# Optimization experiments

Measured on AMD Instinct MI355X. Metric: run time of the kernel, lower is better.

## Reference

```python
import jax, jax.numpy as jnp
import numpy as np

D = H = W = 128
C = 16
VOXEL_SIZE = 0.05  # origin = 0, grid spans [0, 6.4]^3 in world coords
N_POINTS = 2_000_000


def setup_inputs() -> dict:
    key = jax.random.key(0)
    k1, k2 = jax.random.split(key)
    # world-space query points uniformly inside the grid bounds
    points = jax.random.uniform(k1, (N_POINTS, 3), dtype=jnp.float32) * (D * VOXEL_SIZE)
    values = jax.random.normal(k2, (D, H, W, C), dtype=jnp.float32)
    return {"points": points, "values": values}


def reference(points, values):
    # world -> grid coords (origin = 0)
    gc = points / VOXEL_SIZE  # [N, 3]
    x, y, z = gc[:, 0], gc[:, 1], gc[:, 2]

    x0 = jnp.clip(jnp.floor(x).astype(jnp.int32), 0, D - 1)
    y0 = jnp.clip(jnp.floor(y).astype(jnp.int32), 0, H - 1)
    z0 = jnp.clip(jnp.floor(z).astype(jnp.int32), 0, W - 1)
    x1 = jnp.clip(x0 + 1, 0, D - 1)
    y1 = jnp.clip(y0 + 1, 0, H - 1)
    z1 = jnp.clip(z0 + 1, 0, W - 1)

    # fractional offsets (computed against the clipped floor index, as in source)
    xd = (x - x0.astype(x.dtype))[:, None]
    yd = (y - y0.astype(y.dtype))[:, None]
    zd = (z - z0.astype(z.dtype))[:, None]

    # flatten grid for efficient single-axis gather
    flat = values.reshape(D * H * W, C)

    def gather(xi, yi, zi):
        lin = (xi * H + yi) * W + zi  # [N]
        return jnp.take(flat, lin, axis=0)  # [N, C]

    c000 = gather(x0, y0, z0)
    c001 = gather(x0, y0, z1)
    c010 = gather(x0, y1, z0)
    c011 = gather(x0, y1, z1)
    c100 = gather(x1, y0, z0)
    c101 = gather(x1, y0, z1)
    c110 = gather(x1, y1, z0)
    c111 = gather(x1, y1, z1)

    c00 = c000 * (1 - xd) + c100 * xd
    c01 = c001 * (1 - xd) + c101 * xd
    c10 = c010 * (1 - xd) + c110 * xd
    c11 = c011 * (1 - xd) + c111 * xd
    c0 = c00 * (1 - yd) + c10 * yd
    c1 = c01 * (1 - yd) + c11 * yd
    return c0 * (1 - zd) + c1 * zd  # [N, C]
```

## Files before the change

### kernel.cpp

```cpp
#include <hip/hip_runtime.h>


#define DD 128
#define HH 128
#define WW 128
#define NBX 16
#define NB (NBX * NBX * NBX)
#define NPART 4
#define CAP2 152
#define CUR_STRIDE 16

typedef float fvec4 __attribute__((ext_vector_type(4)));

__device__ __forceinline__ float4 lerp4(float4 a, float4 b, float t) {
    return make_float4(fmaf(b.x - a.x, t, a.x),
                       fmaf(b.y - a.y, t, a.y),
                       fmaf(b.z - a.z, t, a.z),
                       fmaf(b.w - a.w, t, a.w));
}

__device__ __forceinline__ int clampi(int v, int lo, int hi) {
    return min(max(v, lo), hi);
}

__device__ __forceinline__ float4 trilerp_point(const float4* __restrict__ values,
                                                float x, float y, float z, int c4) {
    float fx = floorf(x), fy = floorf(y), fz = floorf(z);
    int x0 = clampi((int)fx, 0, DD - 1);
    int y0 = clampi((int)fy, 0, HH - 1);
    int z0 = clampi((int)fz, 0, WW - 1);
    int x1 = min(x0 + 1, DD - 1);
    int y1 = min(y0 + 1, HH - 1);
    int z1 = min(z0 + 1, WW - 1);

    float xd = x - (float)x0;
    float yd = y - (float)y0;
    float zd = z - (float)z0;

    #define VIDX(xi, yi, zi) ((((((xi) << 7) + (yi)) << 7) + (zi)) * 4 + c4)
    float4 c000 = values[VIDX(x0, y0, z0)];
    float4 c001 = values[VIDX(x0, y0, z1)];
    float4 c010 = values[VIDX(x0, y1, z0)];
    float4 c011 = values[VIDX(x0, y1, z1)];
    float4 c100 = values[VIDX(x1, y0, z0)];
    float4 c101 = values[VIDX(x1, y0, z1)];
    float4 c110 = values[VIDX(x1, y1, z0)];
    float4 c111 = values[VIDX(x1, y1, z1)];
    #undef VIDX

    float4 c00 = lerp4(c000, c100, xd);
    float4 c01 = lerp4(c001, c101, xd);
    float4 c10 = lerp4(c010, c110, xd);
    float4 c11 = lerp4(c011, c111, xd);
    float4 c0  = lerp4(c00, c10, yd);
    float4 c1  = lerp4(c01, c11, yd);
    return lerp4(c0, c1, zd);
}

__global__ __launch_bounds__(256) void scatter_kernel(
    const float* __restrict__ points,
    unsigned* __restrict__ cursors,
    float4* __restrict__ recs,
    const float4* __restrict__ values,
    float4* __restrict__ out,
    int n_points)
{
    int p = blockIdx.x * blockDim.x + threadIdx.x;
    if (p >= n_points) return;
    int part = blockIdx.x & (NPART - 1);

    float x = points[p * 3 + 0] * 20.0f;
    float y = points[p * 3 + 1] * 20.0f;
    float z = points[p * 3 + 2] * 20.0f;

    int bx = clampi((int)floorf(x), 0, DD - 1) >> 3;
    int by = clampi((int)floorf(y), 0, HH - 1) >> 3;
    int bz = clampi((int)floorf(z), 0, WW - 1) >> 3;
    int sb = (part * NB) + ((bx * NBX + by) * NBX + bz);

    unsigned pos = atomicAdd(&cursors[sb * CUR_STRIDE], 1u);
    if (pos < CAP2) {
        fvec4 r = { x, y, z, __uint_as_float((unsigned)p) };
        __builtin_nontemporal_store(r, (fvec4*)(recs + (size_t)sb * CAP2 + pos));
    } else {
        #pragma unroll
        for (int c = 0; c < 4; ++c)
            out[p * 4 + c] = trilerp_point(values, x, y, z, c);
    }
}

__global__ __launch_bounds__(256) void interp_kernel(
    const float4* __restrict__ recs,
    const unsigned* __restrict__ cursors,
    const float4* __restrict__ values,
    float4* __restrict__ out)
{
    __shared__ float4 sv[9 * 9 * 9 * 4];

    int b = blockIdx.x;
    int bz = b & 15, by = (b >> 4) & 15, bx = b >> 8;
    int X0 = bx << 3, Y0 = by << 3, Z0 = bz << 3;

    for (int e = threadIdx.x; e < 9 * 9 * 9 * 4; e += 256) {
        int v = e >> 2, c = e & 3;
        int i = v / 81;
        int r = v - i * 81;
        int j = r / 9;
        int k = r - j * 9;
        int gx = min(X0 + i, DD - 1);
        int gy = min(Y0 + j, HH - 1);
        int gz = min(Z0 + k, WW - 1);
        sv[e] = values[((((gx << 7) + gy) << 7) + gz) * 4 + c];
    }
    __syncthreads();

    int c4 = threadIdx.x & 3;

    #define SIDX(i, j, k) (((((i) * 9) + (j)) * 9 + (k)) * 4 + c4)
    for (int part = 0; part < NPART; ++part) {
        int sb = part * NB + b;
        unsigned cnt = cursors[sb * CUR_STRIDE];
        if (cnt > CAP2) cnt = CAP2;
        const float4* rp = recs + (size_t)sb * CAP2;

        for (unsigned j = threadIdx.x >> 2; j < cnt; j += 64) {
            float4 r = rp[j];
            float x = r.x, y = r.y, z = r.z;

            float fx = floorf(x), fy = floorf(y), fz = floorf(z);
            int x0 = clampi((int)fx, 0, DD - 1);
            int y0 = clampi((int)fy, 0, HH - 1);
            int z0 = clampi((int)fz, 0, WW - 1);
            float xd = x - (float)x0;
            float yd = y - (float)y0;
            float zd = z - (float)z0;

            int xl = x0 - X0, yl = y0 - Y0, zl = z0 - Z0;
            float4 c000 = sv[SIDX(xl,     yl,     zl    )];
            float4 c001 = sv[SIDX(xl,     yl,     zl + 1)];
            float4 c010 = sv[SIDX(xl,     yl + 1, zl    )];
            float4 c011 = sv[SIDX(xl,     yl + 1, zl + 1)];
            float4 c100 = sv[SIDX(xl + 1, yl,     zl    )];
            float4 c101 = sv[SIDX(xl + 1, yl,     zl + 1)];
            float4 c110 = sv[SIDX(xl + 1, yl + 1, zl    )];
            float4 c111 = sv[SIDX(xl + 1, yl + 1, zl + 1)];

            float4 c00 = lerp4(c000, c100, xd);
            float4 c01 = lerp4(c001, c101, xd);
            float4 c10 = lerp4(c010, c110, xd);
            float4 c11 = lerp4(c011, c111, xd);
            float4 c0  = lerp4(c00, c10, yd);
            float4 c1  = lerp4(c01, c11, yd);
            float4 res = lerp4(c0, c1, zd);

            unsigned idx = __float_as_uint(r.w);
            __builtin_nontemporal_store(*(fvec4*)&res, (fvec4*)(out + ((size_t)idx * 4 + c4)));
        }
    }
    #undef SIDX
}

__global__ __launch_bounds__(256) void trilerp_kernel(
    const float* __restrict__ points,
    const float4* __restrict__ values,
    float4* __restrict__ out,
    int n_points)
{
    int t = blockIdx.x * blockDim.x + threadIdx.x;
    int p = t >> 2;
    int c4 = t & 3;
    if (p >= n_points) return;

    float x = points[p * 3 + 0] * 20.0f;
    float y = points[p * 3 + 1] * 20.0f;
    float z = points[p * 3 + 2] * 20.0f;
    out[t] = trilerp_point(values, x, y, z, c4);
}

extern "C" void kernel_launch(void* const* d_in, const int* in_sizes, int n_in,
                              void* d_out, int out_size, void* d_ws, size_t ws_size,
                              hipStream_t stream) {
    const float* points = (const float*)d_in[0];
    const float4* values = (const float4*)d_in[1];
    float4* out = (float4*)d_out;

    int n_points = in_sizes[0] / 3;

    const size_t cursors_bytes = (size_t)NPART * NB * CUR_STRIDE * sizeof(unsigned);
    const size_t recs_bytes = (size_t)NPART * NB * CAP2 * sizeof(float4);
    const size_t required = cursors_bytes + recs_bytes;

    if (d_ws != nullptr && ws_size >= required) {
        unsigned* cursors = (unsigned*)d_ws;
        float4* recs = (float4*)((char*)d_ws + cursors_bytes);

        hipMemsetAsync(cursors, 0, cursors_bytes, stream);

        int blocks = (n_points + 255) / 256;
        scatter_kernel<<<blocks, 256, 0, stream>>>(points, cursors, recs, values, out, n_points);
        interp_kernel<<<NB, 256, 0, stream>>>(recs, cursors, values, out);
    } else {
        int total_threads = n_points * 4;
        int blocks = (total_threads + 255) / 256;
        trilerp_kernel<<<blocks, 256, 0, stream>>>(points, values, out, n_points);
    }
}
```

Before: 439.7 us.

## Replace single-pass atomic binning with two-level coarse/fine LDS-staged scatter

Points are now binned in two passes. The first pass sorts them into 64 coarse cells, staging records in shared memory and flushing them in warp-sized batches with a single global atomic per batch. The second pass splits each coarse cell into its 8^3 fine blocks the same way, then the existing per-block interpolation kernel runs on the fine bins. This is meant to cut per-point global atomic contention and scattered record writes, at the cost of an extra pass over the records and an additional kernel launch. It also needs a larger workspace, and when that is not available the code falls back to a direct scatter path.

```diff
diff --git a/kernel.cpp b/kernel.cpp
--- a/kernel.cpp
+++ b/kernel.cpp
@@ -2,13 +2,18 @@
 
 
 #define DD 128
-#define HH 128
-#define WW 128
 #define NBX 16
-#define NB (NBX * NBX * NBX)
-#define NPART 4
-#define CAP2 152
-#define CUR_STRIDE 16
+#define NB  (NBX * NBX * NBX)
+#define NCX 4
+#define NC  (NCX * NCX * NCX)
+#define NFPC 64
+#define CAPC 33000
+#define CAPF 560
+#define CAPL 48
+#define FLUSH_T 32
+#define CCUR_STRIDE 16
+#define FCUR_STRIDE 4
+#define SCAT_BLOCKS 512
 
 typedef float fvec4 __attribute__((ext_vector_type(4)));
 
@@ -27,11 +32,11 @@
                                                 float x, float y, float z, int c4) {
     float fx = floorf(x), fy = floorf(y), fz = floorf(z);
     int x0 = clampi((int)fx, 0, DD - 1);
-    int y0 = clampi((int)fy, 0, HH - 1);
-    int z0 = clampi((int)fz, 0, WW - 1);
+    int y0 = clampi((int)fy, 0, DD - 1);
+    int z0 = clampi((int)fz, 0, DD - 1);
     int x1 = min(x0 + 1, DD - 1);
-    int y1 = min(y0 + 1, HH - 1);
-    int z1 = min(z0 + 1, WW - 1);
+    int y1 = min(y0 + 1, DD - 1);
+    int z1 = min(z0 + 1, DD - 1);
 
     float xd = x - (float)x0;
     float yd = y - (float)y0;
@@ -57,107 +62,281 @@
     return lerp4(c0, c1, zd);
 }
 
-__global__ __launch_bounds__(256) void scatter_kernel(
+__device__ __forceinline__ void write_point_direct(const float4* __restrict__ values,
+                                                   float4* __restrict__ out,
+                                                   float x, float y, float z, unsigned p) {
+    #pragma unroll
+    for (int c = 0; c < 4; ++c)
+        out[(size_t)p * 4 + c] = trilerp_point(values, x, y, z, c);
+}
+
+__global__ __launch_bounds__(256) void coarse_scatter(
     const float* __restrict__ points,
-    unsigned* __restrict__ cursors,
-    float4* __restrict__ recs,
+    unsigned* __restrict__ ccur,
+    float4* __restrict__ crecs,
     const float4* __restrict__ values,
     float4* __restrict__ out,
     int n_points)
 {
+    __shared__ float4 stage[NC * CAPL];
+    __shared__ unsigned scnt[NC];
+
+    for (int i = threadIdx.x; i < NC; i += 256) scnt[i] = 0;
+    __syncthreads();
+
+    int per = (n_points + SCAT_BLOCKS - 1) / SCAT_BLOCKS;
+    int lo = blockIdx.x * per;
+    int hi = min(lo + per, n_points);
+    int lane = threadIdx.x & 63;
+    int wid  = threadIdx.x >> 6;
+
+    for (int base = lo; base < hi; base += 256) {
+        int p = base + threadIdx.x;
+        if (p < hi) {
+            float x = points[p * 3 + 0] * 20.0f;
+            float y = points[p * 3 + 1] * 20.0f;
+            float z = points[p * 3 + 2] * 20.0f;
+            int cx = clampi((int)floorf(x), 0, DD - 1) >> 5;
+            int cy = clampi((int)floorf(y), 0, DD - 1) >> 5;
+            int cz = clampi((int)floorf(z), 0, DD - 1) >> 5;
+            int c = (cx * NCX + cy) * NCX + cz;
+            unsigned pos = atomicAdd(&scnt[c], 1u);
+            if (pos < CAPL) {
+                stage[c * CAPL + pos] = make_float4(x, y, z, __uint_as_float((unsigned)p));
+            } else {
+                unsigned g = atomicAdd(&ccur[c * CCUR_STRIDE], 1u);
+                if (g < CAPC) {
+                    fvec4 r = { x, y, z, __uint_as_float((unsigned)p) };
+                    __builtin_nontemporal_store(r, (fvec4*)(crecs + (size_t)c * CAPC + g));
+                } else {
+                    write_point_direct(values, out, x, y, z, (unsigned)p);
+                }
+            }
+        }
+        __syncthreads();
+        for (int cb = wid * 16; cb < wid * 16 + 16; ++cb) {
+            unsigned cnt = scnt[cb];
+            if (cnt >= FLUSH_T) {
+                unsigned wcnt = cnt < CAPL ? cnt : (unsigned)CAPL;
+                unsigned gb = 0;
+                if (lane == 0) gb = atomicAdd(&ccur[cb * CCUR_STRIDE], wcnt);
+                gb = __shfl(gb, 0);
+                if (lane < (int)wcnt) {
+                    float4 r = stage[cb * CAPL + lane];
+                    unsigned g = gb + (unsigned)lane;
+                    if (g < CAPC)
+                        __builtin_nontemporal_store(*(fvec4*)&r, (fvec4*)(crecs + (size_t)cb * CAPC + g));
+                    else
+                        write_point_direct(values, out, r.x, r.y, r.z, __float_as_uint(r.w));
+                }
+                if (lane == 0) scnt[cb] = 0;
+            }
+        }
+        __syncthreads();
+    }
+    for (int cb = wid * 16; cb < wid * 16 + 16; ++cb) {
+        unsigned cnt = scnt[cb];
+        if (cnt > 0) {
+            unsigned wcnt = cnt < CAPL ? cnt : (unsigned)CAPL;
+            unsigned gb = 0;
+            if (lane == 0) gb = atomicAdd(&ccur[cb * CCUR_STRIDE], wcnt);
+            gb = __shfl(gb, 0);
+            if (lane < (int)wcnt) {
+                float4 r = stage[cb * CAPL + lane];
+                unsigned g = gb + (unsigned)lane;
+                if (g < CAPC)
+                    __builtin_nontemporal_store(*(fvec4*)&r, (fvec4*)(crecs + (size_t)cb * CAPC + g));
+                else
+                    write_point_direct(values, out, r.x, r.y, r.z, __float_as_uint(r.w));
+            }
+        }
+    }
+}
+
+__global__ __launch_bounds__(256) void fine_scatter(
+    const float4* __restrict__ crecs,
+    const unsigned* __restrict__ ccur,
+    unsigned* __restrict__ fcur,
+    float4* __restrict__ frecs,
+    const float4* __restrict__ values,
+    float4* __restrict__ out)
+{
+    __shared__ float4 stage[NFPC * CAPL];
+    __shared__ unsigned scnt[NFPC];
+
+    for (int i = threadIdx.x; i < NFPC; i += 256) scnt[i] = 0;
+    __syncthreads();
+
+    int c   = blockIdx.x >> 3;
+    int sub = blockIdx.x & 7;
+    int cx = c >> 4, cy = (c >> 2) & 3, cz = c & 3;
+    unsigned total = ccur[c * CCUR_STRIDE];
+    if (total > CAPC) total = CAPC;
+    unsigned slo = (unsigned)(((unsigned long long)total * (unsigned)sub) >> 3);
+    unsigned shi = (unsigned)(((unsigned long long)total * (unsigned)(sub + 1)) >> 3);
+    const float4* src = crecs + (size_t)c * CAPC;
+    int lane = threadIdx.x & 63;
+    int wid  = threadIdx.x >> 6;
+
+    for (unsigned base = slo; base < shi; base += 256) {
+        unsigned i = base + threadIdx.x;
+        if (i < shi) {
+            float4 r = src[i];
+            int fx = clampi((int)floorf(r.x), 0, DD - 1) >> 3;
+            int fy = clampi((int)floorf(r.y), 0, DD - 1) >> 3;
+            int fz = clampi((int)floorf(r.z), 0, DD - 1) >> 3;
+            int lf = ((fx & 3) * 4 + (fy & 3)) * 4 + (fz & 3);
+            unsigned pos = atomicAdd(&scnt[lf], 1u);
+            if (pos < CAPL) {
+                stage[lf * CAPL + pos] = r;
+            } else {
+                int fb = (fx * NBX + fy) * NBX + fz;
+                unsigned g = atomicAdd(&fcur[fb * FCUR_STRIDE], 1u);
+                if (g < CAPF)
+                    __builtin_nontemporal_store(*(fvec4*)&r, (fvec4*)(frecs + (size_t)fb * CAPF + g));
+                else
+                    write_point_direct(values, out, r.x, r.y, r.z, __float_as_uint(r.w));
+            }
+        }
+        __syncthreads();
+        for (int lb = wid * 16; lb < wid * 16 + 16; ++lb) {
+            unsigned cnt = scnt[lb];
+            if (cnt >= FLUSH_T) {
+                unsigned wcnt = cnt < CAPL ? cnt : (unsigned)CAPL;
+                int fx = cx * 4 + (lb >> 4);
+                int fy = cy * 4 + ((lb >> 2) & 3);
+                int fz = cz * 4 + (lb & 3);
+                int fb = (fx * NBX + fy) * NBX + fz;
+                unsigned gb = 0;
+                if (lane == 0) gb = atomicAdd(&fcur[fb * FCUR_STRIDE], wcnt);
+                gb = __shfl(gb, 0);
+                if (lane < (int)wcnt) {
+                    float4 r = stage[lb * CAPL + lane];
+                    unsigned g = gb + (unsigned)lane;
+                    if (g < CAPF)
+                        __builtin_nontemporal_store(*(fvec4*)&r, (fvec4*)(frecs + (size_t)fb * CAPF + g));
+                    else
+                        write_point_direct(values, out, r.x, r.y, r.z, __float_as_uint(r.w));
+                }
+                if (lane == 0) scnt[lb] = 0;
+            }
+        }
+        __syncthreads();
+    }
+    for (int lb = wid * 16; lb < wid * 16 + 16; ++lb) {
+        unsigned cnt = scnt[lb];
+        if (cnt > 0) {
+            unsigned wcnt = cnt < CAPL ? cnt : (unsigned)CAPL;
+            int fx = cx * 4 + (lb >> 4);
+            int fy = cy * 4 + ((lb >> 2) & 3);
+            int fz = cz * 4 + (lb & 3);
+            int fb = (fx * NBX + fy) * NBX + fz;
+            unsigned gb = 0;
+            if (lane == 0) gb = atomicAdd(&fcur[fb * FCUR_STRIDE], wcnt);
+            gb = __shfl(gb, 0);
+            if (lane < (int)wcnt) {
+                float4 r = stage[lb * CAPL + lane];
+                unsigned g = gb + (unsigned)lane;
+                if (g < CAPF)
+                    __builtin_nontemporal_store(*(fvec4*)&r, (fvec4*)(frecs + (size_t)fb * CAPF + g));
+                else
+                    write_point_direct(values, out, r.x, r.y, r.z, __float_as_uint(r.w));
+            }
+        }
+    }
+}
+
+__global__ __launch_bounds__(256) void interp_kernel(
+    const float4* __restrict__ recs,
+    const unsigned* __restrict__ fcur,
+    const float4* __restrict__ values,
+    float4* __restrict__ out)
+{
+    __shared__ float4 sv[9 * 9 * 9 * 4];
+
+    int b = blockIdx.x;
+    int bz = b & 15, by = (b >> 4) & 15, bx = b >> 8;
+    int X0 = bx << 3, Y0 = by << 3, Z0 = bz << 3;
+
+    for (int e = threadIdx.x; e < 9 * 9 * 9 * 4; e += 256) {
+        int v = e >> 2, cc = e & 3;
+        int i = v / 81;
+        int rr = v - i * 81;
+        int j = rr / 9;
+        int k = rr - j * 9;
+        int gx = min(X0 + i, DD - 1);
+        int gy = min(Y0 + j, DD - 1);
+        int gz = min(Z0 + k, DD - 1);
+        sv[e] = values[((((gx << 7) + gy) << 7) + gz) * 4 + cc];
+    }
+    __syncthreads();
+
+    int c4 = threadIdx.x & 3;
+    unsigned cnt = fcur[b * FCUR_STRIDE];
+    if (cnt > CAPF) cnt = CAPF;
+    const float4* rp = recs + (size_t)b * CAPF;
+
+    #define SIDX(i, j, k) (((((i) * 9) + (j)) * 9 + (k)) * 4 + c4)
+    for (unsigned j = threadIdx.x >> 2; j < cnt; j += 64) {
+        float4 r = rp[j];
+        float x = r.x, y = r.y, z = r.z;
+
+        float fx = floorf(x), fy = floorf(y), fz = floorf(z);
+        int x0 = clampi((int)fx, 0, DD - 1);
+        int y0 = clampi((int)fy, 0, DD - 1);
+        int z0 = clampi((int)fz, 0, DD - 1);
+        float xd = x - (float)x0;
+        float yd = y - (float)y0;
+        float zd = z - (float)z0;
+
+        int xl = x0 - X0, yl = y0 - Y0, zl = z0 - Z0;
+        float4 c000 = sv[SIDX(xl,     yl,     zl    )];
+        float4 c001 = sv[SIDX(xl,     yl,     zl + 1)];
+        float4 c010 = sv[SIDX(xl,     yl + 1, zl    )];
+        float4 c011 = sv[SIDX(xl,     yl + 1, zl + 1)];
+        float4 c100 = sv[SIDX(xl + 1, yl,     zl    )];
+        float4 c101 = sv[SIDX(xl + 1, yl,     zl + 1)];
+        float4 c110 = sv[SIDX(xl + 1, yl + 1, zl    )];
+        float4 c111 = sv[SIDX(xl + 1, yl + 1, zl + 1)];
+
+        float4 c00 = lerp4(c000, c100, xd);
+        float4 c01 = lerp4(c001, c101, xd);
+        float4 c10 = lerp4(c010, c110, xd);
+        float4 c11 = lerp4(c011, c111, xd);
+        float4 c0  = lerp4(c00, c10, yd);
+        float4 c1  = lerp4(c01, c11, yd);
+        float4 res = lerp4(c0, c1, zd);
+
+        unsigned idx = __float_as_uint(r.w);
+        __builtin_nontemporal_store(*(fvec4*)&res, (fvec4*)(out + ((size_t)idx * 4 + c4)));
+    }
+    #undef SIDX
+}
+
+__global__ __launch_bounds__(256) void direct_scatter(
+    const float* __restrict__ points,
+    unsigned* __restrict__ fcur,
+    float4* __restrict__ frecs,
+    const float4* __restrict__ values,
+    float4* __restrict__ out,
+    int n_points)
+{
     int p = blockIdx.x * blockDim.x + threadIdx.x;
     if (p >= n_points) return;
-    int part = blockIdx.x & (NPART - 1);
-
     float x = points[p * 3 + 0] * 20.0f;
     float y = points[p * 3 + 1] * 20.0f;
     float z = points[p * 3 + 2] * 20.0f;
-
-    int bx = clampi((int)floorf(x), 0, DD - 1) >> 3;
-    int by = clampi((int)floorf(y), 0, HH - 1) >> 3;
-    int bz = clampi((int)floorf(z), 0, WW - 1) >> 3;
-    int sb = (part * NB) + ((bx * NBX + by) * NBX + bz);
-
-    unsigned pos = atomicAdd(&cursors[sb * CUR_STRIDE], 1u);
-    if (pos < CAP2) {
+    int fx = clampi((int)floorf(x), 0, DD - 1) >> 3;
+    int fy = clampi((int)floorf(y), 0, DD - 1) >> 3;
+    int fz = clampi((int)floorf(z), 0, DD - 1) >> 3;
+    int fb = (fx * NBX + fy) * NBX + fz;
+    unsigned pos = atomicAdd(&fcur[fb * FCUR_STRIDE], 1u);
+    if (pos < CAPF) {
         fvec4 r = { x, y, z, __uint_as_float((unsigned)p) };
-        __builtin_nontemporal_store(r, (fvec4*)(recs + (size_t)sb * CAP2 + pos));
+        __builtin_nontemporal_store(r, (fvec4*)(frecs + (size_t)fb * CAPF + pos));
     } else {
-        #pragma unroll
-        for (int c = 0; c < 4; ++c)
-            out[p * 4 + c] = trilerp_point(values, x, y, z, c);
-    }
-}
-
-__global__ __launch_bounds__(256) void interp_kernel(
-    const float4* __restrict__ recs,
-    const unsigned* __restrict__ cursors,
-    const float4* __restrict__ values,
-    float4* __restrict__ out)
-{
-    __shared__ float4 sv[9 * 9 * 9 * 4];
-
-    int b = blockIdx.x;
-    int bz = b & 15, by = (b >> 4) & 15, bx = b >> 8;
-    int X0 = bx << 3, Y0 = by << 3, Z0 = bz << 3;
-
-    for (int e = threadIdx.x; e < 9 * 9 * 9 * 4; e += 256) {
-        int v = e >> 2, c = e & 3;
-        int i = v / 81;
-        int r = v - i * 81;
-        int j = r / 9;
-        int k = r - j * 9;
-        int gx = min(X0 + i, DD - 1);
-        int gy = min(Y0 + j, HH - 1);
-        int gz = min(Z0 + k, WW - 1);
-        sv[e] = values[((((gx << 7) + gy) << 7) + gz) * 4 + c];
-    }
-    __syncthreads();
-
-    int c4 = threadIdx.x & 3;
-
-    #define SIDX(i, j, k) (((((i) * 9) + (j)) * 9 + (k)) * 4 + c4)
-    for (int part = 0; part < NPART; ++part) {
-        int sb = part * NB + b;
-        unsigned cnt = cursors[sb * CUR_STRIDE];
-        if (cnt > CAP2) cnt = CAP2;
-        const float4* rp = recs + (size_t)sb * CAP2;
-
-        for (unsigned j = threadIdx.x >> 2; j < cnt; j += 64) {
-            float4 r = rp[j];
-            float x = r.x, y = r.y, z = r.z;
-
-            float fx = floorf(x), fy = floorf(y), fz = floorf(z);
-            int x0 = clampi((int)fx, 0, DD - 1);
-            int y0 = clampi((int)fy, 0, HH - 1);
-            int z0 = clampi((int)fz, 0, WW - 1);
-            float xd = x - (float)x0;
-            float yd = y - (float)y0;
-            float zd = z - (float)z0;
-
-            int xl = x0 - X0, yl = y0 - Y0, zl = z0 - Z0;
-            float4 c000 = sv[SIDX(xl,     yl,     zl    )];
-            float4 c001 = sv[SIDX(xl,     yl,     zl + 1)];
-            float4 c010 = sv[SIDX(xl,     yl + 1, zl    )];
-            float4 c011 = sv[SIDX(xl,     yl + 1, zl + 1)];
-            float4 c100 = sv[SIDX(xl + 1, yl,     zl    )];
-            float4 c101 = sv[SIDX(xl + 1, yl,     zl + 1)];
-            float4 c110 = sv[SIDX(xl + 1, yl + 1, zl    )];
-            float4 c111 = sv[SIDX(xl + 1, yl + 1, zl + 1)];
-
-            float4 c00 = lerp4(c000, c100, xd);
-            float4 c01 = lerp4(c001, c101, xd);
-            float4 c10 = lerp4(c010, c110, xd);
-            float4 c11 = lerp4(c011, c111, xd);
-            float4 c0  = lerp4(c00, c10, yd);
-            float4 c1  = lerp4(c01, c11, yd);
-            float4 res = lerp4(c0, c1, zd);
-
-            unsigned idx = __float_as_uint(r.w);
-            __builtin_nontemporal_store(*(fvec4*)&res, (fvec4*)(out + ((size_t)idx * 4 + c4)));
-        }
-    }
-    #undef SIDX
+        write_point_direct(values, out, x, y, z, (unsigned)p);
+    }
 }
 
 __global__ __launch_bounds__(256) void trilerp_kernel(
@@ -170,7 +349,6 @@
     int p = t >> 2;
     int c4 = t & 3;
     if (p >= n_points) return;
-
     float x = points[p * 3 + 0] * 20.0f;
     float y = points[p * 3 + 1] * 20.0f;
     float z = points[p * 3 + 2] * 20.0f;
@@ -183,22 +361,31 @@
     const float* points = (const float*)d_in[0];
     const float4* values = (const float4*)d_in[1];
     float4* out = (float4*)d_out;
-
     int n_points = in_sizes[0] / 3;
 
-    const size_t cursors_bytes = (size_t)NPART * NB * CUR_STRIDE * sizeof(unsigned);
-    const size_t recs_bytes = (size_t)NPART * NB * CAP2 * sizeof(float4);
-    const size_t required = cursors_bytes + recs_bytes;
-
-    if (d_ws != nullptr && ws_size >= required) {
-        unsigned* cursors = (unsigned*)d_ws;
-        float4* recs = (float4*)((char*)d_ws + cursors_bytes);
-
-        hipMemsetAsync(cursors, 0, cursors_bytes, stream);
-
+    const size_t ccur_b  = (size_t)NC * CCUR_STRIDE * sizeof(unsigned);
+    const size_t fcur_b  = (size_t)NB * FCUR_STRIDE * sizeof(unsigned);
+    const size_t crecs_b = (size_t)NC * CAPC * sizeof(float4);
+    const size_t frecs_b = (size_t)NB * CAPF * sizeof(float4);
+
+    if (d_ws != nullptr && ws_size >= ccur_b + fcur_b + crecs_b + frecs_b) {
+        unsigned* ccur  = (unsigned*)d_ws;
+        unsigned* fcur  = (unsigned*)((char*)d_ws + ccur_b);
+        float4*   crecs = (float4*)((char*)d_ws + ccur_b + fcur_b);
+        float4*   frecs = (float4*)((char*)d_ws + ccur_b + fcur_b + crecs_b);
+
+        hipMemsetAsync(d_ws, 0, ccur_b + fcur_b, stream);
+        coarse_scatter<<<SCAT_BLOCKS, 256, 0, stream>>>(points, ccur, crecs, values, out, n_points);
+        fine_scatter<<<NC * 8, 256, 0, stream>>>(crecs, ccur, fcur, frecs, values, out);
+        interp_kernel<<<NB, 256, 0, stream>>>(frecs, fcur, values, out);
+    } else if (d_ws != nullptr && ws_size >= fcur_b + frecs_b) {
+        unsigned* fcur  = (unsigned*)d_ws;
+        float4*   frecs = (float4*)((char*)d_ws + fcur_b);
+
+        hipMemsetAsync(d_ws, 0, fcur_b, stream);
         int blocks = (n_points + 255) / 256;
-        scatter_kernel<<<blocks, 256, 0, stream>>>(points, cursors, recs, values, out, n_points);
-        interp_kernel<<<NB, 256, 0, stream>>>(recs, cursors, values, out);
+        direct_scatter<<<blocks, 256, 0, stream>>>(points, fcur, frecs, values, out, n_points);
+        interp_kernel<<<NB, 256, 0, stream>>>(frecs, fcur, values, out);
     } else {
         int total_threads = n_points * 4;
         int blocks = (total_threads + 255) / 256;
```

New measurement: 417.8 us. 1.05x faster.
